# Performance work log

Hardware: AMD Instinct MI355X
Metric: run time of the kernel (lower is better)

## Reference

```python
import jax, jax.numpy as jnp
import numpy as np

B_SZ = 8
G = 2048
D_MODEL = 512
D_STATE = 128
D_CONV = 4
EXPAND = 2
HEADDIM = 64
D_INNER = EXPAND * D_MODEL          # 1024
NHEADS = D_INNER // HEADDIM         # 16
CONV_DIM = D_INNER + 2 * D_STATE    # 1280
D_IN_PROJ = 2 * D_INNER + 2 * D_STATE + NHEADS  # 2320
ID_DIM = 128
CHR_DIM = 64
N_CHR = 25
F_LOCUS = 32
PATH_DIM = 128
GENE_FEAT = ID_DIM + PATH_DIM + 2 * CHR_DIM  # 384
N_PERT = 10000
P_DIM = 128


def silu(x):
    return x * jax.nn.sigmoid(x)


def causal_dw_conv(x, w, b):
    # x: (B,L,C), w: (C,K), b: (C,)  causal depthwise conv (left pad K-1)
    K = w.shape[1]
    L = x.shape[1]
    xp = jnp.pad(x, ((0, 0), (K - 1, 0), (0, 0)))
    out = b[None, None, :]
    for k in range(K):
        out = out + xp[:, k:k + L, :] * w[:, k][None, None, :]
    return out


def mamba2(u, in_w, conv_w, conv_b, dt_bias, A_log, Dp, norm_w, out_w):
    # u: (B,L,d_model) -> (B,L,d_model); mamba_ssm Mamba2 defaults, ngroups=1
    Bb, L, _ = u.shape
    zxbcdt = u @ in_w.T                                   # (B,L,D_IN_PROJ)
    z = zxbcdt[..., :D_INNER]
    xBC = zxbcdt[..., D_INNER:D_INNER + CONV_DIM]
    dt = zxbcdt[..., D_INNER + CONV_DIM:]                 # (B,L,H)
    xBC = silu(causal_dw_conv(xBC, conv_w, conv_b))
    x = xBC[..., :D_INNER].reshape(Bb, L, NHEADS, HEADDIM)
    Bm = xBC[..., D_INNER:D_INNER + D_STATE]              # (B,L,N)
    Cm = xBC[..., D_INNER + D_STATE:]                     # (B,L,N)
    dt = jax.nn.softplus(dt + dt_bias)                    # (B,L,H)
    dA = jnp.exp(dt * (-jnp.exp(A_log)))                  # (B,L,H)

    def step(h, inp):
        dA_t, dt_t, B_t, C_t, x_t = inp
        h = dA_t[:, :, None, None] * h + jnp.einsum('bh,bn,bhp->bhpn', dt_t, B_t, x_t)
        y = jnp.einsum('bhpn,bn->bhp', h, C_t)
        return h, y

    h0 = jnp.zeros((Bb, NHEADS, HEADDIM, D_STATE), u.dtype)
    xs = (dA.transpose(1, 0, 2), dt.transpose(1, 0, 2),
          Bm.transpose(1, 0, 2), Cm.transpose(1, 0, 2), x.transpose(1, 0, 2, 3))
    _, ys = jax.lax.scan(step, h0, xs)                    # ys: (L,B,H,P)
    y = ys.transpose(1, 0, 2, 3) + Dp[None, None, :, None] * x
    y = y.reshape(Bb, L, D_INNER)
    # gated RMSNorm (norm_before_gate=False): norm(y * silu(z))
    y = y * silu(z)
    y = y * jax.lax.rsqrt(jnp.mean(y * y, axis=-1, keepdims=True) + 1e-5) * norm_w
    return y @ out_w.T


def setup_inputs() -> dict:
    key = jax.random.key(0)
    ks = iter(jax.random.split(key, 48))

    def nrm(shape, scale):
        return jax.random.normal(next(ks), shape, jnp.float32) * scale

    inp = {}
    inp['perturbation_idx'] = jax.random.randint(next(ks), (B_SZ,), 0, N_PERT)
    inp['chr_idx'] = jax.random.randint(next(ks), (G,), 0, N_CHR)
    inp['locus_fourier'] = nrm((G, 2 * F_LOCUS), 1.0)
    inp['pathway_features'] = nrm((G, PATH_DIM), 1.0)
    inp['pert_emb'] = nrm((N_PERT, P_DIM), 0.02)
    inp['gene_id_emb'] = nrm((G, ID_DIM), 0.02)
    inp['chr_emb'] = nrm((N_CHR, CHR_DIM), 0.02)
    inp['locus_w'] = nrm((CHR_DIM, 2 * F_LOCUS), (2 * F_LOCUS) ** -0.5)
    inp['locus_b'] = jnp.zeros((CHR_DIM,), jnp.float32)
    inp['cond_w'] = nrm((GENE_FEAT, P_DIM), P_DIM ** -0.5)
    inp['cond_b'] = jnp.zeros((GENE_FEAT,), jnp.float32)
    inp['in_w'] = nrm((D_MODEL, GENE_FEAT), GENE_FEAT ** -0.5)
    inp['in_b'] = jnp.zeros((D_MODEL,), jnp.float32)
    inp['head_w'] = nrm((1, D_MODEL), D_MODEL ** -0.5)
    inp['head_b'] = jnp.zeros((1,), jnp.float32)
    for p in ('f_', 'b_'):
        inp[p + 'in_w'] = nrm((D_IN_PROJ, D_MODEL), D_MODEL ** -0.5)
        inp[p + 'conv_w'] = nrm((CONV_DIM, D_CONV), D_CONV ** -0.5)
        inp[p + 'conv_b'] = jnp.zeros((CONV_DIM,), jnp.float32)
        inp[p + 'dt_bias'] = nrm((NHEADS,), 0.5)
        inp[p + 'A_log'] = jnp.log(jax.random.uniform(next(ks), (NHEADS,), jnp.float32, 1.0, 16.0))
        inp[p + 'D'] = jnp.ones((NHEADS,), jnp.float32)
        inp[p + 'norm_w'] = jnp.ones((D_INNER,), jnp.float32)
        inp[p + 'out_w'] = nrm((D_MODEL, D_INNER), D_INNER ** -0.5)
    return inp


def reference(perturbation_idx, chr_idx, locus_fourier, pathway_features,
              pert_emb, gene_id_emb, chr_emb, locus_w, locus_b,
              cond_w, cond_b, in_w, in_b, head_w, head_b,
              f_in_w, f_conv_w, f_conv_b, f_dt_bias, f_A_log, f_D, f_norm_w, f_out_w,
              b_in_w, b_conv_w, b_conv_b, b_dt_bias, b_A_log, b_D, b_norm_w, b_out_w):
    B = perturbation_idx.shape[0]
    cond = pert_emb[perturbation_idx] @ cond_w.T + cond_b          # (B, GENE_FEAT)
    e_chr = chr_emb[chr_idx]                                        # (G, CHR_DIM)
    e_locus = jax.nn.gelu(locus_fourier @ locus_w.T + locus_b, approximate=False)
    gene_feat = jnp.concatenate([gene_id_emb, pathway_features, e_chr, e_locus], axis=1)  # (G, GENE_FEAT)
    seq = jnp.concatenate([cond[:, None, :],
                           jnp.broadcast_to(gene_feat[None], (B,) + gene_feat.shape)], axis=1)
    seq = seq @ in_w.T + in_b                                       # (B, G+1, d_model)
    h_fwd = mamba2(seq, f_in_w, f_conv_w, f_conv_b, f_dt_bias, f_A_log, f_D, f_norm_w, f_out_w)
    h_bwd = jnp.flip(mamba2(jnp.flip(seq, axis=1), b_in_w, b_conv_w, b_conv_b,
                            b_dt_bias, b_A_log, b_D, b_norm_w, b_out_w), axis=1)
    H = h_fwd + h_bwd
    return H[:, 1:, :] @ head_w.T + head_b                          # (B, G, 1)
```

## Files before the change

### kernel.cpp

```cpp
#include <hip/hip_runtime.h>
#include <hip/hip_bf16.h>
#include <hip/hip_fp16.h>
#include <math.h>

#define DPROJ 2320
#define CONVD 1280

typedef __attribute__((ext_vector_type(8))) short bf16x8;
typedef __attribute__((ext_vector_type(4))) float f32x4;

__device__ __forceinline__ float siluf(float x) { return x / (1.f + __expf(-x)); }
__device__ __forceinline__ float bfu(unsigned short s) { return __uint_as_float(((unsigned)s) << 16); }
__device__ __forceinline__ unsigned short f2bf(float f) {
    unsigned u = __float_as_uint(f);
    unsigned r = (u + 0x7FFFu + ((u >> 16) & 1u)) >> 16;
    return (unsigned short)r;
}
__device__ __forceinline__ unsigned short f2h(float f) {
    __half h = __float2half(f);
    return *(unsigned short*)&h;
}
__device__ __forceinline__ float h2f(unsigned short s) {
    __half h = *(__half*)&s;
    return __half2float(h);
}


__global__ void gg_kernel(const int* __restrict__ chridx, const float* __restrict__ gid,
                          const float* __restrict__ path, const float* __restrict__ chrE,
                          const int* __restrict__ pidx, const float* __restrict__ pertE,
                          float* __restrict__ gf, float* __restrict__ cemb,
                          float* __restrict__ wf2, float* __restrict__ wb2) {
    int blk = blockIdx.x, tid = threadIdx.x;
    if (blk < 3072) {
        int idx = blk * 256 + tid;
        int g = idx / 384, j = idx % 384;
        float v;
        if (j < 128)      v = gid[(size_t)g * 128 + j];
        else if (j < 256) v = path[(size_t)g * 128 + (j - 128)];
        else if (j < 320) v = chrE[(size_t)chridx[g] * 64 + (j - 256)];
        else return;
        gf[idx] = v;
    } else if (blk < 3076) {
        int idx = (blk - 3072) * 256 + tid;
        int b = idx >> 7, k = idx & 127;
        cemb[idx] = pertE[(size_t)pidx[b] * 128 + k];
    } else {
        wf2[tid * 4 + 0] = 0.f; wf2[tid * 4 + 1] = 0.f;
        wf2[tid * 4 + 2] = 0.f; wf2[tid * 4 + 3] = 0.f;
        wb2[tid * 4 + 0] = 0.f; wb2[tid * 4 + 1] = 0.f;
        wb2[tid * 4 + 2] = 0.f; wb2[tid * 4 + 3] = 0.f;
    }
}

__global__ void wfold_kernel(const float* __restrict__ headW,
                             const float* __restrict__ fOutW, const float* __restrict__ fNw,
                             const float* __restrict__ bOutW, const float* __restrict__ bNw,
                             float* __restrict__ wf2, float* __restrict__ wb2) {
    int blk = blockIdx.x;
    int dir = blk >> 6;
    int rem = blk & 63;
    int dseg = rem >> 4, mseg = rem & 15;
    int tid = threadIdx.x;
    int d = dseg * 256 + tid;
    const float* W = dir ? bOutW : fOutW;
    float s = 0.f;
#pragma unroll
    for (int m = mseg * 32; m < mseg * 32 + 32; ++m)
        s += headW[m] * W[(size_t)m * 1024 + d];
    const float* nw = dir ? bNw : fNw;
    atomicAdd(&(dir ? wb2 : wf2)[d], s * nw[d]);
}


__global__ void tobf4_kernel(const float* __restrict__ inW, const float* __restrict__ fInW,
                             const float* __restrict__ bInW, const float* __restrict__ gf,
                             unsigned short* __restrict__ inW2, unsigned short* __restrict__ fInW2,
                             unsigned short* __restrict__ bInW2, unsigned short* __restrict__ gf2) {
    size_t idx = (size_t)blockIdx.x * 256 + threadIdx.x;
    const size_t A = 512UL * 384, B5 = 2432UL * 512;
    if (idx < A) {
        inW2[idx] = f2bf(inW[idx]);
    } else if (idx < A + B5) {
        size_t k = idx - A; int m = k / 512, kk = k % 512;
        fInW2[k] = f2bf(m < 2320 ? fInW[(size_t)m * 512 + kk] : 0.f);
    } else if (idx < A + 2 * B5) {
        size_t k = idx - A - B5; int m = k / 512, kk = k % 512;
        bInW2[k] = f2bf(m < 2320 ? bInW[(size_t)m * 512 + kk] : 0.f);
    } else {
        size_t k = idx - A - 2 * B5;
        gf2[k] = f2bf(gf[k]);
    }
}


__global__ __launch_bounds__(256) void mfma_gemm_kernel(
    const unsigned short* __restrict__ A2, const unsigned short* __restrict__ W2,
    const float* __restrict__ bias, unsigned short* __restrict__ Cbf,
    int N, int K2, int ldc) {
    __shared__ __align__(16) unsigned short Al[128 * 40];
    __shared__ __align__(16) unsigned short Bl[128 * 40];
    const int tid = threadIdx.x;
    const int bm = blockIdx.y * 128, bn = blockIdx.x * 128;
    const int lane = tid & 63, wave = tid >> 6;
    const int wm = (wave >> 1) * 64, wn = (wave & 1) * 64;
    f32x4 acc[4][4];
#pragma unroll
    for (int i = 0; i < 4; ++i)
#pragma unroll
        for (int j = 0; j < 4; ++j) acc[i][j] = (f32x4){0.f, 0.f, 0.f, 0.f};

    for (int k0 = 0; k0 < K2; k0 += 32) {
        __syncthreads();
#pragma unroll
        for (int s = 0; s < 2; ++s) {
            int ch = tid + 256 * s;
            int row = ch >> 2, q = ch & 3;
            uint4 va = *(const uint4*)&A2[(size_t)(bm + row) * K2 + k0 + q * 8];
            *(uint4*)&Al[row * 40 + q * 8] = va;
            uint4 vb = *(const uint4*)&W2[(size_t)(bn + row) * K2 + k0 + q * 8];
            *(uint4*)&Bl[row * 40 + q * 8] = vb;
        }
        __syncthreads();
        bf16x8 af[4], bfr[4];
#pragma unroll
        for (int i = 0; i < 4; ++i)
            af[i] = *(const bf16x8*)&Al[(wm + i * 16 + (lane & 15)) * 40 + (lane >> 4) * 8];
#pragma unroll
        for (int j = 0; j < 4; ++j)
            bfr[j] = *(const bf16x8*)&Bl[(wn + j * 16 + (lane & 15)) * 40 + (lane >> 4) * 8];
#pragma unroll
        for (int i = 0; i < 4; ++i)
#pragma unroll
            for (int j = 0; j < 4; ++j)
                acc[i][j] = __builtin_amdgcn_mfma_f32_16x16x32_bf16(af[i], bfr[j], acc[i][j], 0, 0, 0);
    }
#pragma unroll
    for (int i = 0; i < 4; ++i) {
        int m = bm + wm + i * 16 + (lane >> 4) * 4;
#pragma unroll
        for (int j = 0; j < 4; ++j) {
            int n = bn + wn + j * 16 + (lane & 15);
            if (n < N) {
                float bv = bias ? bias[n] : 0.f;
#pragma unroll
                for (int r = 0; r < 4; ++r)
                    Cbf[(size_t)(m + r) * ldc + n] = f2bf(acc[i][j][r] + bv);
            }
        }
    }
}


__global__ __launch_bounds__(256) void zx_gemm_kernel(
    const unsigned short* __restrict__ A2,
    const unsigned short* __restrict__ fInW2, const unsigned short* __restrict__ bInW2,
    unsigned short* __restrict__ szF, unsigned short* __restrict__ xbcF, float* __restrict__ dtrF,
    unsigned short* __restrict__ szB, unsigned short* __restrict__ xbcB, float* __restrict__ dtrB) {
    __shared__ __align__(16) unsigned short Al[128 * 40];
    __shared__ __align__(16) unsigned short Bl[128 * 40];
    const int tid = threadIdx.x;
    const int bxx = blockIdx.x;
    const int d = (bxx >= 19);
    const int bn = (d ? bxx - 19 : bxx) * 128, bm = blockIdx.y * 128;
    const unsigned short* W2 = d ? bInW2 : fInW2;
    unsigned short* sz = d ? szB : szF;
    unsigned short* xbc = d ? xbcB : xbcF;
    float* dtr = d ? dtrB : dtrF;
    const int lane = tid & 63, wave = tid >> 6;
    const int wm = (wave >> 1) * 64, wn = (wave & 1) * 64;
    const int K2 = 512, N = 2320;
    f32x4 acc[4][4];
#pragma unroll
    for (int i = 0; i < 4; ++i)
#pragma unroll
        for (int j = 0; j < 4; ++j) acc[i][j] = (f32x4){0.f, 0.f, 0.f, 0.f};

    for (int k0 = 0; k0 < K2; k0 += 32) {
        __syncthreads();
#pragma unroll
        for (int s = 0; s < 2; ++s) {
            int ch = tid + 256 * s;
            int row = ch >> 2, q = ch & 3;
            uint4 va = *(const uint4*)&A2[(size_t)(bm + row) * K2 + k0 + q * 8];
            *(uint4*)&Al[row * 40 + q * 8] = va;
            uint4 vb = *(const uint4*)&W2[(size_t)(bn + row) * K2 + k0 + q * 8];
            *(uint4*)&Bl[row * 40 + q * 8] = vb;
        }
        __syncthreads();
        bf16x8 af[4], bfr[4];
#pragma unroll
        for (int i = 0; i < 4; ++i)
            af[i] = *(const bf16x8*)&Al[(wm + i * 16 + (lane & 15)) * 40 + (lane >> 4) * 8];
#pragma unroll
        for (int j = 0; j < 4; ++j)
            bfr[j] = *(const bf16x8*)&Bl[(wn + j * 16 + (lane & 15)) * 40 + (lane >> 4) * 8];
#pragma unroll
        for (int i = 0; i < 4; ++i)
#pragma unroll
            for (int j = 0; j < 4; ++j)
                acc[i][j] = __builtin_amdgcn_mfma_f32_16x16x32_bf16(af[i], bfr[j], acc[i][j], 0, 0, 0);
    }
#pragma unroll
    for (int i = 0; i < 4; ++i) {
        int m = bm + wm + i * 16 + (lane >> 4) * 4;
#pragma unroll
        for (int j = 0; j < 4; ++j) {
            int n = bn + wn + j * 16 + (lane & 15);
            if (n < N) {
#pragma unroll
                for (int r = 0; r < 4; ++r) {
                    float v = acc[i][j][r];
                    if (n < 1024)
                        sz[(size_t)(m + r) * 1024 + n] = f2h(siluf(v));
                    else if (n < 2304)
                        xbc[(size_t)(m + r) * 1280 + (n - 1024)] = f2bf(v);
                    else
                        dtr[(size_t)(m + r) * 16 + (n - 2304)] = v;
                }
            }
        }
    }
}


__global__ __launch_bounds__(256) void gemm_kernel(
    const float* __restrict__ A, const float* __restrict__ W,
    const float* __restrict__ bias, float* __restrict__ C,
    int M, int N, int K, int ldc, int act) {
    __shared__ __align__(16) float As[16][68];
    __shared__ __align__(16) float Ws[16][68];
    const int tid = threadIdx.x;
    const int tx = tid & 15, ty = tid >> 4;
    const int bm = blockIdx.y * 64, bn = blockIdx.x * 64;
    const int lr = tid >> 2;
    const int lk = (tid & 3) * 4;
    float acc[4][4];
#pragma unroll
    for (int i = 0; i < 4; ++i)
#pragma unroll
        for (int j = 0; j < 4; ++j) acc[i][j] = 0.f;

    for (int k0 = 0; k0 < K; k0 += 16) {
        const int am = bm + lr;
        const int wn = bn + lr;
        float4 av = make_float4(0.f, 0.f, 0.f, 0.f), wv = make_float4(0.f, 0.f, 0.f, 0.f);
        if (am < M) av = *(const float4*)&A[(size_t)am * K + k0 + lk];
        if (wn < N) wv = *(const float4*)&W[(size_t)wn * K + k0 + lk];
        __syncthreads();
        As[lk + 0][lr] = av.x; As[lk + 1][lr] = av.y; As[lk + 2][lr] = av.z; As[lk + 3][lr] = av.w;
        Ws[lk + 0][lr] = wv.x; Ws[lk + 1][lr] = wv.y; Ws[lk + 2][lr] = wv.z; Ws[lk + 3][lr] = wv.w;
        __syncthreads();
#pragma unroll
        for (int kk = 0; kk < 16; ++kk) {
            float4 a = *(const float4*)&As[kk][ty * 4];
            float4 w = *(const float4*)&Ws[kk][tx * 4];
            float aa[4] = {a.x, a.y, a.z, a.w}, ww[4] = {w.x, w.y, w.z, w.w};
#pragma unroll
            for (int i = 0; i < 4; ++i)
#pragma unroll
                for (int j = 0; j < 4; ++j) acc[i][j] += aa[i] * ww[j];
        }
    }
#pragma unroll
    for (int i = 0; i < 4; ++i) {
        const int m = bm + ty * 4 + i;
        if (m >= M) continue;
#pragma unroll
        for (int j = 0; j < 4; ++j) {
            const int n = bn + tx * 4 + j;
            if (n >= N) continue;
            float v = acc[i][j] + (bias ? bias[n] : 0.f);
            if (act == 1) v = 0.5f * v * (1.f + erff(v * 0.70710678118654752f));
            C[(size_t)m * ldc + n] = v;
        }
    }
}


__global__ void dt_kernel(const float* __restrict__ dtrF, const float* __restrict__ dtrB,
                          const float* __restrict__ zxc,
                          const float* __restrict__ fDtB, const float* __restrict__ bDtB,
                          float* __restrict__ dtFsT, float* __restrict__ dtBsT,
                          float* __restrict__ dtFp) {
    int idx = blockIdx.x * 256 + threadIdx.x;
    if (idx < 32768) {
        int r = idx >> 4, hh = idx & 15;
        float raw = dtrF[idx] + fDtB[hh];
        dtFsT[hh * 2048 + r] = (raw > 20.f) ? raw : log1pf(expf(raw));
    } else if (idx < 65536) {
        int k = idx - 32768;
        int r = k >> 4, hh = k & 15;
        float raw = dtrB[(size_t)(2047 - r) * 16 + hh] + bDtB[hh];
        dtBsT[hh * 2048 + r] = (raw > 20.f) ? raw : log1pf(expf(raw));
    } else if (idx < 65664) {
        int k = idx - 65536;
        int b = k >> 4, hh = k & 15;
        float raw = zxc[(size_t)b * DPROJ + 2304 + hh] + fDtB[hh];
        dtFp[k] = (raw > 20.f) ? raw : log1pf(expf(raw));
    }
}

__global__ void cum_kernel(const float* __restrict__ dtFsT, const float* __restrict__ dtBsT,
                           const float* __restrict__ fAlog, const float* __restrict__ bAlog,
                           float* __restrict__ cumF, float* __restrict__ cumB) {
    int id = blockIdx.x * 256 + threadIdx.x;
    int dir = id >> 9, k = id & 511, h = k >> 5, c = k & 31;
    const float* dtT = dir ? dtBsT : dtFsT;
    const float* Al = dir ? bAlog : fAlog;
    float* cum = dir ? cumB : cumF;
    float a = -expf(Al[h]);
    float acc = 0.f;
    for (int s4 = 0; s4 < 16; ++s4) {
        float4 v = *(const float4*)&dtT[h * 2048 + c * 64 + s4 * 4];
        float4 o;
        acc += v.x * a; o.x = acc;
        acc += v.y * a; o.y = acc;
        acc += v.z * a; o.z = acc;
        acc += v.w * a; o.w = acc;
        *(float4*)&cum[h * 2048 + c * 64 + s4 * 4] = o;
    }
}


__global__ void conv_kernel(const unsigned short* __restrict__ xbcF,
                            const unsigned short* __restrict__ xbcB,
                            const float* __restrict__ zxc,
                            const float* __restrict__ fCw, const float* __restrict__ fCb,
                            const float* __restrict__ bCw, const float* __restrict__ bCb,
                            unsigned short* __restrict__ bcF, unsigned short* __restrict__ xF16,
                            unsigned short* __restrict__ bcB, unsigned short* __restrict__ xB16,
                            float* __restrict__ convFp, unsigned short* __restrict__ bcFp,
                            unsigned short* __restrict__ xFp16) {
    int blk = blockIdx.x, tid = threadIdx.x;
    if (blk < 10225) {
        int idx = blk * 256 + tid;
        if (idx >= 2045 * 1280) return;
        int t4 = idx / 1280, c = idx % 1280;
        float4 w4 = *(const float4*)&fCw[c * 4];
        float acc = fCb[c];
        acc += bfu(xbcF[(size_t)(t4 + 0) * 1280 + c]) * w4.x;
        acc += bfu(xbcF[(size_t)(t4 + 1) * 1280 + c]) * w4.y;
        acc += bfu(xbcF[(size_t)(t4 + 2) * 1280 + c]) * w4.z;
        acc += bfu(xbcF[(size_t)(t4 + 3) * 1280 + c]) * w4.w;
        float r = siluf(acc);
        if (c >= 1024) bcF[(size_t)t4 * 256 + (c - 1024)] = f2bf(r);
        else           xF16[(size_t)t4 * 1024 + c] = f2bf(r);
    } else if (blk < 20465) {
        int idx = (blk - 10225) * 256 + tid;
        int s = idx / 1280, c = idx % 1280;
        float4 w4 = *(const float4*)&bCw[c * 4];
        float w[4] = {w4.x, w4.y, w4.z, w4.w};
        float acc = bCb[c];
#pragma unroll
        for (int k = 0; k < 4; ++k) {
            int j = s - 3 + k;
            if (j >= 0) acc += bfu(xbcB[(size_t)(2047 - j) * 1280 + c]) * w[k];
        }
        float r = siluf(acc);
        if (c >= 1024) bcB[(size_t)s * 256 + (c - 1024)] = f2bf(r);
        else           xB16[(size_t)s * 1024 + c] = f2bf(r);
    } else {
        int idx = (blk - 20465) * 256 + tid;
        int b = idx / 5120;
        int r = idx % 5120;
        int t = r / 1280, c = r % 1280;
        float4 w4 = *(const float4*)&fCw[c * 4];
        float w[4] = {w4.x, w4.y, w4.z, w4.w};
        float acc = fCb[c];
#pragma unroll
        for (int k = 0; k < 4; ++k) {
            int j = t - 3 + k;
            float x = 0.f;
            if (j == 0)      x = zxc[(size_t)b * DPROJ + 1024 + c];
            else if (j >= 1) x = bfu(xbcF[(size_t)(j - 1) * 1280 + c]);
            acc += x * w[k];
        }
        float rr = siluf(acc);
        convFp[idx] = rr;
        if (c >= 1024) bcFp[(size_t)(b * 4 + t) * 256 + (c - 1024)] = f2bf(rr);
        else           xFp16[(size_t)(b * 4 + t) * 1024 + c] = f2bf(rr);
    }
}


__global__ __launch_bounds__(256) void intra_kernel(
    const unsigned short* __restrict__ bcF, const unsigned short* __restrict__ bcFp,
    const unsigned short* __restrict__ bcB,
    const unsigned short* __restrict__ xF16, const unsigned short* __restrict__ xFp16,
    const unsigned short* __restrict__ xB16,
    const float* __restrict__ dtFsT, const float* __restrict__ dtBsT,
    const float* __restrict__ cumF, const float* __restrict__ cumB,
    unsigned short* __restrict__ YiF0, unsigned short* __restrict__ YiFs,
    unsigned short* __restrict__ YiB,
    unsigned short* __restrict__ UF0, unsigned short* __restrict__ UFs,
    unsigned short* __restrict__ UB) {
    __shared__ __align__(16) unsigned char smraw[63232];
    unsigned short* Bt = (unsigned short*)smraw;
    unsigned short* Ct = (unsigned short*)(smraw + 17408);
    unsigned short* Sm = (unsigned short*)(smraw + 17408);
    unsigned short* BT = (unsigned short*)(smraw + 34816);
    unsigned short* XT = (unsigned short*)(smraw + 53248);
    float* scum = (float*)(smraw + 62464);
    float* sdt  = scum + 64;
    float* se   = scum + 128;

    const int iid = blockIdx.x;
    int dir, b = 0, h, c;
    unsigned short *Yout, *Uout;
    if (iid < 128)      { dir = 0; b = iid >> 4; h = iid & 15; c = 0;
                          Yout = YiF0 + (size_t)(b * 16 + h) * 4096; Uout = UF0 + (size_t)(b * 16 + h) * 8192; }
    else if (iid < 624) { int k = iid - 128; dir = 0; c = 1 + (k >> 4); h = k & 15;
                          Yout = YiFs + (size_t)(c * 16 + h) * 4096; Uout = UFs + (size_t)(c * 16 + h) * 8192; }
    else                { int k = iid - 624; dir = 1; c = k >> 4; h = k & 15;
                          Yout = YiB + (size_t)(c * 16 + h) * 4096;  Uout = UB + (size_t)(c * 16 + h) * 8192; }
    const float* dtAT = dir ? dtBsT : dtFsT;
    const float* cumA = dir ? cumB : cumF;

    const int tid = threadIdx.x;
    const int lane = tid & 63, wave = tid >> 6;
    const int quad = lane >> 4, l15 = lane & 15;

    {
        int r = tid >> 2, q = tid & 3;
        const unsigned short *bsrc, *xsrc;
        if (dir == 0) {
            int t = 64 * c + 1 + r;
            if (t < 4) { bsrc = bcFp + (size_t)(b * 4 + t) * 256; xsrc = xFp16 + (size_t)(b * 4 + t) * 1024; }
            else       { bsrc = bcF + (size_t)(t - 4) * 256;      xsrc = xF16 + (size_t)(t - 4) * 1024; }
        } else {
            int s = 64 * c + r;
            bsrc = bcB + (size_t)s * 256;
            xsrc = xB16 + (size_t)s * 1024;
        }
#pragma unroll
        for (int i = 0; i < 4; ++i) {
            int n0 = q * 32 + i * 8;
            uint4 v = *(const uint4*)&bsrc[n0];
            *(uint4*)&Bt[r * 136 + n0] = v;
            const unsigned short* pv = (const unsigned short*)&v;
#pragma unroll
            for (int jj = 0; jj < 8; ++jj) BT[(n0 + jj) * 72 + r] = pv[jj];
        }
#pragma unroll
        for (int i = 0; i < 4; ++i) {
            int n0 = q * 32 + i * 8;
            uint4 v = *(const uint4*)&bsrc[128 + n0];
            *(uint4*)&Ct[r * 136 + n0] = v;
        }
#pragma unroll
        for (int k = 0; k < 2; ++k) {
            uint4 v = *(const uint4*)&xsrc[h * 64 + q * 16 + k * 8];
            const unsigned short* pv = (const unsigned short*)&v;
#pragma unroll
            for (int jj = 0; jj < 8; ++jj) XT[(q * 16 + k * 8 + jj) * 72 + r] = pv[jj];
        }
        if (tid < 64) {
            int j = 64 * c + tid;
            scum[tid] = cumA[h * 2048 + j];
            sdt[tid] = dtAT[h * 2048 + j];
        }
    }
    __syncthreads();
    if (tid < 64) se[tid] = __expf(scum[63] - scum[tid]) * sdt[tid];

    const int tm = (wave >> 1) * 32, sn = (wave & 1) * 32;
    f32x4 acc1[2][2];
#pragma unroll
    for (int i = 0; i < 2; ++i)
#pragma unroll
        for (int j = 0; j < 2; ++j) acc1[i][j] = (f32x4){0.f, 0.f, 0.f, 0.f};
#pragma unroll
    for (int ks = 0; ks < 4; ++ks) {
        bf16x8 af[2], bfr[2];
#pragma unroll
        for (int i = 0; i < 2; ++i)
            af[i] = *(const bf16x8*)&Ct[(tm + i * 16 + l15) * 136 + ks * 32 + quad * 8];
#pragma unroll
        for (int j = 0; j < 2; ++j)
            bfr[j] = *(const bf16x8*)&Bt[(sn + j * 16 + l15) * 136 + ks * 32 + quad * 8];
#pragma unroll
        for (int i = 0; i < 2; ++i)
#pragma unroll
            for (int j = 0; j < 2; ++j)
                acc1[i][j] = __builtin_amdgcn_mfma_f32_16x16x32_bf16(af[i], bfr[j], acc1[i][j], 0, 0, 0);
    }
    __syncthreads();

#pragma unroll
    for (int j = 0; j < 2; ++j) {
        int s = sn + j * 16 + l15;
        float cs = scum[s], ds = sdt[s];
#pragma unroll
        for (int i = 0; i < 2; ++i) {
#pragma unroll
            for (int r = 0; r < 4; ++r) {
                int t = tm + i * 16 + quad * 4 + r;
                float v = (s <= t) ? __expf(scum[t] - cs) * ds * acc1[i][j][r] : 0.f;
                Sm[t * 72 + s] = f2bf(v);
            }
        }
    }
    __syncthreads();

    const int pm = (wave >> 1) * 32, tn = (wave & 1) * 32;
    f32x4 acc2[2][2];
#pragma unroll
    for (int i = 0; i < 2; ++i)
#pragma unroll
        for (int j = 0; j < 2; ++j) acc2[i][j] = (f32x4){0.f, 0.f, 0.f, 0.f};
#pragma unroll
    for (int ks = 0; ks < 2; ++ks) {
        bf16x8 af[2], bfr[2];
#pragma unroll
        for (int i = 0; i < 2; ++i)
            af[i] = *(const bf16x8*)&XT[(pm + i * 16 + l15) * 72 + ks * 32 + quad * 8];
#pragma unroll
        for (int j = 0; j < 2; ++j)
            bfr[j] = *(const bf16x8*)&Sm[(tn + j * 16 + l15) * 72 + ks * 32 + quad * 8];
#pragma unroll
        for (int i = 0; i < 2; ++i)
#pragma unroll
            for (int j = 0; j < 2; ++j)
                acc2[i][j] = __builtin_amdgcn_mfma_f32_16x16x32_bf16(af[i], bfr[j], acc2[i][j], 0, 0, 0);
    }
#pragma unroll
    for (int i = 0; i < 2; ++i)
#pragma unroll
        for (int j = 0; j < 2; ++j) {
            int t = tn + j * 16 + l15;
            int p0 = pm + i * 16 + quad * 4;
            ushort4 o = make_ushort4(f2bf(acc2[i][j][0]), f2bf(acc2[i][j][1]),
                                     f2bf(acc2[i][j][2]), f2bf(acc2[i][j][3]));
            *(ushort4*)&Yout[t * 64 + p0] = o;
        }

    const int nm = wave * 32;
    f32x4 acc3[2][4];
#pragma unroll
    for (int i = 0; i < 2; ++i)
#pragma unroll
        for (int j = 0; j < 4; ++j) acc3[i][j] = (f32x4){0.f, 0.f, 0.f, 0.f};
#pragma unroll
    for (int ks = 0; ks < 2; ++ks) {
        float ev[8];
#pragma unroll
        for (int jj = 0; jj < 8; ++jj) ev[jj] = se[ks * 32 + quad * 8 + jj];
        bf16x8 bfx[4];
#pragma unroll
        for (int j = 0; j < 4; ++j) {
            bf16x8 xs = *(const bf16x8*)&XT[(j * 16 + l15) * 72 + ks * 32 + quad * 8];
#pragma unroll
            for (int jj = 0; jj < 8; ++jj)
                bfx[j][jj] = (short)f2bf(bfu((unsigned short)xs[jj]) * ev[jj]);
        }
        bf16x8 af[2];
#pragma unroll
        for (int i = 0; i < 2; ++i)
            af[i] = *(const bf16x8*)&BT[(nm + i * 16 + l15) * 72 + ks * 32 + quad * 8];
#pragma unroll
        for (int i = 0; i < 2; ++i)
#pragma unroll
            for (int j = 0; j < 4; ++j)
                acc3[i][j] = __builtin_amdgcn_mfma_f32_16x16x32_bf16(af[i], bfx[j], acc3[i][j], 0, 0, 0);
    }
#pragma unroll
    for (int i = 0; i < 2; ++i)
#pragma unroll
        for (int j = 0; j < 4; ++j) {
            int p = j * 16 + l15;
            int n0 = nm + i * 16 + quad * 4;
            ushort4 o = make_ushort4(f2bf(acc3[i][j][0]), f2bf(acc3[i][j][1]),
                                     f2bf(acc3[i][j][2]), f2bf(acc3[i][j][3]));
            *(ushort4*)&Uout[p * 128 + n0] = o;
        }
}


__global__ void mid_kernel(const float* __restrict__ convFp, const unsigned short* __restrict__ bcF,
                           const float* __restrict__ dtFp, const float* __restrict__ cumF,
                           const float* __restrict__ cumB,
                           const unsigned short* __restrict__ UF0,
                           const unsigned short* __restrict__ UFs, const unsigned short* __restrict__ UB,
                           float* __restrict__ cb0, unsigned short* __restrict__ Mb,
                           unsigned short* __restrict__ Tst, float* __restrict__ psiF) {
    int blk = blockIdx.x, tid = threadIdx.x;
    if (blk < 32) {
        int idx = blk * 256 + tid;
        int b = idx >> 10, r = idx & 1023, h = r >> 6, tl = r & 63;
        int t = tl + 1;
        const float* b0 = convFp + (size_t)(b * 4) * CONVD;
        float s = 0.f;
        if (t < 4) {
            const float* crow = convFp + (size_t)(b * 4 + t) * CONVD;
            for (int n = 0; n < 128; ++n) s += crow[1152 + n] * b0[1024 + n];
        } else {
            const unsigned short* cr = bcF + (size_t)(t - 4) * 256 + 128;
            for (int n = 0; n < 128; ++n) s += bfu(cr[n]) * b0[1024 + n];
        }
        cb0[(b * 16 + h) * 64 + tl] = s * dtFp[b * 16 + h];
    } else if (blk < 160) {
        int bh = blk - 32;
        int b = bh >> 4, h = bh & 15;
        float D0 = __expf(cumF[h * 2048 + 63]);
        float dt0 = dtFp[b * 16 + h];
        const float* row0 = convFp + (size_t)(b * 4) * CONVD;
        const unsigned short* u = UF0 + (size_t)(b * 16 + h) * 8192;
        unsigned short* m = Mb + (size_t)(b * 16 + h) * 8192;
        for (int e4 = tid; e4 < 2048; e4 += 256) {
            int e = e4 * 4, p = e >> 7, n0 = e & 127;
            float s = D0 * dt0 * row0[h * 64 + p];
            float4 B4 = *(const float4*)&row0[1024 + n0];
            ushort4 uv = *(const ushort4*)&u[e];
            ushort4 o = make_ushort4(f2bf(s * B4.x + bfu(uv.x)), f2bf(s * B4.y + bfu(uv.y)),
                                     f2bf(s * B4.z + bfu(uv.z)), f2bf(s * B4.w + bfu(uv.w)));
            *(ushort4*)&m[e] = o;
        }
    } else {
        int blk2 = blk - 160;
        int dir = blk2 >> 7, h = (blk2 >> 3) & 15, q8 = blk2 & 7;
        const unsigned short* U = dir ? UB : UFs;
        const float* cum = dir ? cumB : cumF;
        unsigned short* T = Tst + (size_t)(dir * 16 + h) * 32 * 8192;
        if (dir == 0 && q8 == 0 && tid == 0) {
            float ps = 1.f;
            for (int c = 1; c < 32; ++c) {
                psiF[h * 32 + c] = ps;
                ps *= __expf(cumF[h * 2048 + c * 64 + 63]);
            }
        }
        const size_t e = (size_t)q8 * 1024 + 4 * tid;
        float4 st = make_float4(0.f, 0.f, 0.f, 0.f);
        const int c0 = dir ? 0 : 1;
        ushort4 u = *(const ushort4*)&U[((size_t)c0 * 16 + h) * 8192 + e];
        for (int c = c0; c < 32; ++c) {
            ushort4 un = make_ushort4(0, 0, 0, 0);
            if (c + 1 < 32) un = *(const ushort4*)&U[((size_t)(c + 1) * 16 + h) * 8192 + e];
            float Dc = __expf(cum[h * 2048 + c * 64 + 63]);
            ushort4 o = make_ushort4(f2bf(st.x), f2bf(st.y), f2bf(st.z), f2bf(st.w));
            *(ushort4*)&T[(size_t)c * 8192 + e] = o;
            st.x = Dc * st.x + bfu(u.x);
            st.y = Dc * st.y + bfu(u.y);
            st.z = Dc * st.z + bfu(u.z);
            st.w = Dc * st.w + bfu(u.w);
            u = un;
        }
    }
}


__global__ __launch_bounds__(256) void yt_kernel(
    const unsigned short* __restrict__ bcF, const unsigned short* __restrict__ bcB,
    const unsigned short* __restrict__ Tst,
    const unsigned short* __restrict__ YiFs, const unsigned short* __restrict__ YiB,
    const float* __restrict__ cumF, const float* __restrict__ cumB,
    unsigned short* __restrict__ YsF, unsigned short* __restrict__ YsB) {
    const int iid = blockIdx.x;
    int dir, h, c;
    if (iid < 496) { dir = 0; c = 1 + (iid >> 4); h = iid & 15; }
    else           { int k = iid - 496; dir = 1; c = k >> 4; h = k & 15; }
    const unsigned short* Cbase = (dir == 0)
        ? bcF + ((size_t)(64 * c - 3)) * 256 + 128
        : bcB + ((size_t)(64 * c)) * 256 + 128;
    const unsigned short* Tp = Tst + ((size_t)(dir * 16 + h) * 32 + c) * 8192;
    const unsigned short* Yi = (dir == 0 ? YiFs : YiB) + (size_t)(c * 16 + h) * 4096;
    const float* cum = dir ? cumB : cumF;
    unsigned short* Ys = (dir == 0 ? YsF : YsB) + (size_t)(c * 16 + h) * 4096;
    const int tid = threadIdx.x;
    const int lane = tid & 63, wave = tid >> 6;
    const int quad = lane >> 4, l15 = lane & 15;
    const int pm = (wave >> 1) * 32, tb = (wave & 1) * 32;
    f32x4 acc[2][2];
#pragma unroll
    for (int i = 0; i < 2; ++i)
#pragma unroll
        for (int j = 0; j < 2; ++j) acc[i][j] = (f32x4){0.f, 0.f, 0.f, 0.f};
#pragma unroll
    for (int ks = 0; ks < 4; ++ks) {
        bf16x8 af[2], bfr[2];
#pragma unroll
        for (int i = 0; i < 2; ++i)
            af[i] = *(const bf16x8*)&Tp[(size_t)(pm + i * 16 + l15) * 128 + ks * 32 + quad * 8];
#pragma unroll
        for (int j = 0; j < 2; ++j)
            bfr[j] = *(const bf16x8*)&Cbase[(size_t)(tb + j * 16 + l15) * 256 + ks * 32 + quad * 8];
#pragma unroll
        for (int i = 0; i < 2; ++i)
#pragma unroll
            for (int j = 0; j < 2; ++j)
                acc[i][j] = __builtin_amdgcn_mfma_f32_16x16x32_bf16(af[i], bfr[j], acc[i][j], 0, 0, 0);
    }
#pragma unroll
    for (int i = 0; i < 2; ++i)
#pragma unroll
        for (int j = 0; j < 2; ++j) {
            int t = tb + j * 16 + l15;
            int p0 = pm + i * 16 + quad * 4;
            float et = __expf(cum[h * 2048 + 64 * c + t]);
            ushort4 yi = *(const ushort4*)&Yi[t * 64 + p0];
            ushort4 o = make_ushort4(f2bf(bfu(yi.x) + et * acc[i][j][0]),
                                     f2bf(bfu(yi.y) + et * acc[i][j][1]),
                                     f2bf(bfu(yi.z) + et * acc[i][j][2]),
                                     f2bf(bfu(yi.w) + et * acc[i][j][3]));
            *(ushort4*)&Ys[t * 64 + p0] = o;
        }
}


__global__ __launch_bounds__(256) void gate_kernel(
    const unsigned short* __restrict__ bcF,
    const unsigned short* __restrict__ Mb, const float* __restrict__ psiF,
    const unsigned short* __restrict__ YsF, const unsigned short* __restrict__ YsB,
    const unsigned short* __restrict__ xF16, const unsigned short* __restrict__ xFp16,
    const unsigned short* __restrict__ xB16,
    const unsigned short* __restrict__ szF, const unsigned short* __restrict__ szB,
    const float* __restrict__ convFp,
    const float* __restrict__ cumF,
    const unsigned short* __restrict__ YiF0,
    const float* __restrict__ cb0,
    const float* __restrict__ fD, const float* __restrict__ bD,
    const float* __restrict__ wf2, const float* __restrict__ wb2,
    float* __restrict__ aF, float* __restrict__ aB) {
    __shared__ __align__(16) float Ysm[64 * 68];

    const int iid = blockIdx.x;
    int dir, b = 0, h, cg;
    if (iid < 1024) { dir = 0; b = iid >> 7; int r = iid & 127; h = r >> 3; cg = r & 7; }
    else            { int k = iid - 1024; dir = 1; h = k >> 3; cg = k & 7; }
    const int tid = threadIdx.x, tx = tid & 15, ty = tid >> 4;
    const int lane = tid & 63, wave = tid >> 6;
    const int quad = lane >> 4, l15 = lane & 15;

    const float Dh = (dir ? bD : fD)[h];
    const float* wvp = dir ? wb2 : wf2;
    float4 wreg = *(const float4*)&wvp[h * 64 + tx * 4];

    const int pm = (wave >> 1) * 32, tb = (wave & 1) * 32;
    bf16x8 mfr[4][2];
    if (dir == 0) {
        const unsigned short* Mp = Mb + (size_t)(b * 16 + h) * 8192;
#pragma unroll
        for (int ks = 0; ks < 4; ++ks)
#pragma unroll
            for (int i = 0; i < 2; ++i)
                mfr[ks][i] = *(const bf16x8*)&Mp[(size_t)(pm + i * 16 + l15) * 128 + ks * 32 + quad * 8];
    }

    for (int cc = 0; cc < 4; ++cc) {
        const int c = cg * 4 + cc;
        const bool fwdG = (dir == 0 && c > 0);
        if (fwdG) {
            if (cc > 0) __syncthreads();
            const unsigned short* Cbase = bcF + ((size_t)(64 * c - 3)) * 256 + 128;
            f32x4 acc[2][2];
#pragma unroll
            for (int i = 0; i < 2; ++i)
#pragma unroll
                for (int j = 0; j < 2; ++j) acc[i][j] = (f32x4){0.f, 0.f, 0.f, 0.f};
#pragma unroll
            for (int ks = 0; ks < 4; ++ks) {
                bf16x8 bfr[2];
#pragma unroll
                for (int j = 0; j < 2; ++j)
                    bfr[j] = *(const bf16x8*)&Cbase[(size_t)(tb + j * 16 + l15) * 256 + ks * 32 + quad * 8];
#pragma unroll
                for (int i = 0; i < 2; ++i)
#pragma unroll
                    for (int j = 0; j < 2; ++j)
                        acc[i][j] = __builtin_amdgcn_mfma_f32_16x16x32_bf16(mfr[ks][i], bfr[j], acc[i][j], 0, 0, 0);
            }
#pragma unroll
            for (int i = 0; i < 2; ++i)
#pragma unroll
                for (int j = 0; j < 2; ++j)
                    *(f32x4*)&Ysm[(tb + j * 16 + l15) * 68 + pm + i * 16 + quad * 4] = acc[i][j];
            __syncthreads();
        }

        const float psi = fwdG ? psiF[h * 32 + c] : 0.f;
        float4 x0v = make_float4(0.f, 0.f, 0.f, 0.f);
        float cbv[4] = {0.f, 0.f, 0.f, 0.f};
        if (dir == 0 && c == 0) {
            x0v = *(const float4*)&convFp[(size_t)(b * 4) * CONVD + h * 64 + tx * 4];
#pragma unroll
            for (int i = 0; i < 4; ++i) cbv[i] = cb0[(b * 16 + h) * 64 + (ty + 16 * i)];
        }

        float rawet[4];
        ushort4 y4a[4], x4a[4], z4a[4];
        float4 cm4a[4];
#pragma unroll
        for (int i = 0; i < 4; ++i) {
            int tl = ty + 16 * i;
            int j = 64 * c + tl;
            rawet[i] = (dir == 0) ? cumF[h * 2048 + j] : 0.f;
            const unsigned short *Yp, *xp, *zp;
            if (dir == 0) {
                Yp = (c == 0) ? YiF0 + (size_t)(b * 16 + h) * 4096 : YsF + (size_t)(c * 16 + h) * 4096;
                if (c == 0) {
                    int t = j + 1;
                    xp = (t < 4) ? xFp16 + (size_t)(b * 4 + t) * 1024 : xF16 + (size_t)(t - 4) * 1024;
                } else {
                    xp = xF16 + (size_t)(64 * c + tl - 3) * 1024;
                }
                zp = szF + (size_t)j * 1024;
            } else {
                Yp = YsB + (size_t)(c * 16 + h) * 4096;
                xp = xB16 + (size_t)j * 1024;
                zp = szB + (size_t)(2047 - j) * 1024;
            }
            y4a[i] = *(const ushort4*)&Yp[tl * 64 + tx * 4];
            x4a[i] = *(const ushort4*)&xp[h * 64 + tx * 4];
            z4a[i] = *(const ushort4*)&zp[h * 64 + tx * 4];
            if (fwdG)                    cm4a[i] = *(const float4*)&Ysm[tl * 68 + tx * 4];
            else if (dir == 0 && c == 0) cm4a[i] = x0v;
            else                         cm4a[i] = make_float4(0.f, 0.f, 0.f, 0.f);
        }

#pragma unroll
        for (int i = 0; i < 4; ++i) {
            int j = 64 * c + ty + 16 * i;
            float k1 = 0.f;
            if (dir == 0) {
                float et = __expf(rawet[i]);
                k1 = (c == 0) ? et * cbv[i] : et * psi;
            }
            float yv[4] = {bfu(y4a[i].x), bfu(y4a[i].y), bfu(y4a[i].z), bfu(y4a[i].w)};
            float xa[4] = {bfu(x4a[i].x), bfu(x4a[i].y), bfu(x4a[i].z), bfu(x4a[i].w)};
            float sza[4] = {h2f(z4a[i].x), h2f(z4a[i].y), h2f(z4a[i].z), h2f(z4a[i].w)};
            float cma[4] = {cm4a[i].x, cm4a[i].y, cm4a[i].z, cm4a[i].w};
            float wa[4] = {wreg.x, wreg.y, wreg.z, wreg.w};
            float a1 = 0.f, a2 = 0.f;
#pragma unroll
            for (int w = 0; w < 4; ++w) {
                float tot = yv[w] + k1 * cma[w] + Dh * xa[w];
                float g = tot * sza[w];
                a1 += g * wa[w];
                a2 += g * g;
            }
#pragma unroll
            for (int m = 1; m < 16; m <<= 1) {
                a1 += __shfl_xor(a1, m);
                a2 += __shfl_xor(a2, m);
            }
            if (tx == 0) {
                if (dir == 0) {
                    size_t o = ((size_t)(b * 2048 + j) * 16 + h) * 2;
                    aF[o] = a1; aF[o + 1] = a2;
                } else {
                    int g = 2047 - j;
                    size_t o = ((size_t)g * 16 + h) * 2;
                    aB[o] = a1; aB[o + 1] = a2;
                }
            }
        }
    }
}


__global__ void final_kernel(const float* __restrict__ aF, const float* __restrict__ aB,
                             const float* __restrict__ headB, float* __restrict__ out) {
    int idx = blockIdx.x * 256 + threadIdx.x;
    int b = idx >> 11, g = idx & 2047;
    const float* pf = aF + ((size_t)(b * 2048 + g)) * 32;
    const float* pb = aB + (size_t)g * 32;
    float f1 = 0.f, f2 = 0.f, b1 = 0.f, b2 = 0.f;
#pragma unroll
    for (int h = 0; h < 16; ++h) {
        f1 += pf[2 * h]; f2 += pf[2 * h + 1];
        b1 += pb[2 * h]; b2 += pb[2 * h + 1];
    }
    out[idx] = f1 * rsqrtf(f2 * (1.f / 1024.f) + 1e-5f) +
               b1 * rsqrtf(b2 * (1.f / 1024.f) + 1e-5f) + headB[0];
}


extern "C" void kernel_launch(void* const* d_in, const int* in_sizes, int n_in,
                              void* d_out, int out_size, void* d_ws, size_t ws_size,
                              hipStream_t stream) {
    const int*   pidx   = (const int*)  d_in[0];
    const int*   chridx = (const int*)  d_in[1];
    const float* locusF = (const float*)d_in[2];
    const float* pathF  = (const float*)d_in[3];
    const float* pertE  = (const float*)d_in[4];
    const float* gidE   = (const float*)d_in[5];
    const float* chrE   = (const float*)d_in[6];
    const float* locusW = (const float*)d_in[7];
    const float* locusB = (const float*)d_in[8];
    const float* condW  = (const float*)d_in[9];
    const float* condB  = (const float*)d_in[10];
    const float* inW    = (const float*)d_in[11];
    const float* inB    = (const float*)d_in[12];
    const float* headW  = (const float*)d_in[13];
    const float* headB  = (const float*)d_in[14];
    const float* fInW   = (const float*)d_in[15];
    const float* fCw    = (const float*)d_in[16];
    const float* fCb    = (const float*)d_in[17];
    const float* fDtB   = (const float*)d_in[18];
    const float* fAlog  = (const float*)d_in[19];
    const float* fDp    = (const float*)d_in[20];
    const float* fNw    = (const float*)d_in[21];
    const float* fOutW  = (const float*)d_in[22];
    const float* bInW   = (const float*)d_in[23];
    const float* bCw    = (const float*)d_in[24];
    const float* bCb    = (const float*)d_in[25];
    const float* bDtB   = (const float*)d_in[26];
    const float* bAlog  = (const float*)d_in[27];
    const float* bDp    = (const float*)d_in[28];
    const float* bNw    = (const float*)d_in[29];
    const float* bOutW  = (const float*)d_in[30];
    float* out = (float*)d_out;
    (void)in_sizes; (void)n_in; (void)out_size; (void)ws_size;

    char* base = (char*)d_ws;
    size_t off = 0;
    auto allocf = [&](size_t n) -> float* {
        char* r = base + off; off += ((n * 4 + 63) & ~(size_t)63); return (float*)r; };
    auto allocu = [&](size_t n) -> unsigned short* {
        char* r = base + off; off += ((n * 2 + 63) & ~(size_t)63); return (unsigned short*)r; };

    float* gf     = allocf(2048UL * 384);
    float* cond   = allocf(8UL * 384);
    float* cemb   = allocf(8UL * 128);
    float* uc     = allocf(8UL * 512);
    float* zxc    = allocf(8UL * DPROJ);
    float* convFp = allocf(8UL * 4 * CONVD);
    float* dtrF   = allocf(2048UL * 16);
    float* dtrB   = allocf(2048UL * 16);
    float* dtFsT  = allocf(16UL * 2048);
    float* dtFp   = allocf(128);
    float* dtBsT  = allocf(16UL * 2048);
    float* cumF   = allocf(16UL * 2048);
    float* cumB   = allocf(16UL * 2048);
    float* wf2    = allocf(1024);
    float* wb2    = allocf(1024);
    float* cb0    = allocf(8UL * 16 * 64);
    float* psiF   = allocf(16UL * 32);
    float* aF     = allocf(8UL * 2048 * 16 * 2);
    float* aB     = allocf(2048UL * 16 * 2);
    unsigned short* xbcF = allocu(2048UL * 1280);
    unsigned short* xbcB = allocu(2048UL * 1280);
    unsigned short* YiF0 = allocu(8UL * 16 * 4096);
    unsigned short* YiFs = allocu(32UL * 16 * 4096);
    unsigned short* YiB  = allocu(32UL * 16 * 4096);
    unsigned short* UF0  = allocu(8UL * 16 * 8192);
    unsigned short* UFs  = allocu(32UL * 16 * 8192);
    unsigned short* UB   = allocu(32UL * 16 * 8192);
    unsigned short* Mb   = allocu(8UL * 16 * 8192);
    unsigned short* Tst  = allocu(2UL * 16 * 32 * 8192);
    unsigned short* bcF  = allocu(2045UL * 256);
    unsigned short* bcFp = allocu(32UL * 256);
    unsigned short* bcB  = allocu(2048UL * 256);
    unsigned short* YsF  = allocu(32UL * 16 * 4096);
    unsigned short* YsB  = allocu(32UL * 16 * 4096);
    unsigned short* xF16 = allocu(2045UL * 1024);
    unsigned short* xFp16= allocu(32UL * 1024);
    unsigned short* xB16 = allocu(2048UL * 1024);
    unsigned short* szF  = allocu(2048UL * 1024);
    unsigned short* szB  = allocu(2048UL * 1024);
    unsigned short* gf2   = allocu(2048UL * 384);
    unsigned short* inW2  = allocu(512UL * 384);
    unsigned short* ug2   = allocu(2048UL * 512);
    unsigned short* fInW2 = allocu(2432UL * 512);
    unsigned short* bInW2 = allocu(2432UL * 512);

    gg_kernel<<<3077, 256, 0, stream>>>(chridx, gidE, pathF, chrE, pidx, pertE, gf, cemb, wf2, wb2);
    wfold_kernel<<<128, 256, 0, stream>>>(headW, fOutW, fNw, bOutW, bNw, wf2, wb2);
    gemm_kernel<<<dim3(1, 32), 256, 0, stream>>>(locusF, locusW, locusB, gf + 320, 2048, 64, 64, 384, 1);
    gemm_kernel<<<dim3(6, 1), 256, 0, stream>>>(cemb, condW, condB, cond, 8, 384, 128, 384, 0);

    tobf4_kernel<<<13568, 256, 0, stream>>>(inW, fInW, bInW, gf, inW2, fInW2, bInW2, gf2);

    mfma_gemm_kernel<<<dim3(4, 16), 256, 0, stream>>>(gf2, inW2, inB, ug2, 512, 384, 512);
    gemm_kernel<<<dim3(8, 1), 256, 0, stream>>>(cond, inW, inB, uc, 8, 512, 384, 512, 0);

    zx_gemm_kernel<<<dim3(38, 16), 256, 0, stream>>>(ug2, fInW2, bInW2,
                                                     szF, xbcF, dtrF, szB, xbcB, dtrB);
    gemm_kernel<<<dim3(37, 1), 256, 0, stream>>>(uc, fInW, nullptr, zxc, 8, DPROJ, 512, DPROJ, 0);

    dt_kernel<<<257, 256, 0, stream>>>(dtrF, dtrB, zxc, fDtB, bDtB, dtFsT, dtBsT, dtFp);
    cum_kernel<<<4, 256, 0, stream>>>(dtFsT, dtBsT, fAlog, bAlog, cumF, cumB);
    conv_kernel<<<20625, 256, 0, stream>>>(xbcF, xbcB, zxc, fCw, fCb, bCw, bCb,
                                           bcF, xF16, bcB, xB16, convFp, bcFp, xFp16);
    intra_kernel<<<1136, 256, 0, stream>>>(bcF, bcFp, bcB, xF16, xFp16, xB16,
                                           dtFsT, dtBsT, cumF, cumB,
                                           YiF0, YiFs, YiB, UF0, UFs, UB);
    mid_kernel<<<416, 256, 0, stream>>>(convFp, bcF, dtFp, cumF, cumB, UF0, UFs, UB,
                                        cb0, Mb, Tst, psiF);
    yt_kernel<<<1008, 256, 0, stream>>>(bcF, bcB, Tst, YiFs, YiB, cumF, cumB, YsF, YsB);
    gate_kernel<<<1152, 256, 0, stream>>>(bcF, Mb, psiF, YsF, YsB, xF16, xFp16, xB16,
                                          szF, szB, convFp, cumF,
                                          YiF0, cb0, fDp, bDp, wf2, wb2, aF, aB);
    final_kernel<<<64, 256, 0, stream>>>(aF, aB, headB, out);
}
```

Measured before the change: 372.9 us.

## Fold D*x skip term into yt_kernel and split gate_kernel into more blocks

The D*x skip contribution for batch-independent chunks (all backward chunks and forward chunks c>0) is now added once in yt_kernel, which is shared across the batch. gate_kernel no longer re-reads x for those chunks in every batch. gate_kernel also processes 2 chunks per block instead of 4, doubling the grid to 2304 blocks, and issues its global loads before the MFMA/LDS phase so their latency can overlap. Tradeoffs are an extra bf16 rounding of the combined term, since it is folded in before the store, and more per-block setup such as the M fragment loads being repeated.

```diff
diff --git a/kernel.cpp b/kernel.cpp
--- a/kernel.cpp
+++ b/kernel.cpp
@@ -653,7 +653,9 @@
     const unsigned short* __restrict__ bcF, const unsigned short* __restrict__ bcB,
     const unsigned short* __restrict__ Tst,
     const unsigned short* __restrict__ YiFs, const unsigned short* __restrict__ YiB,
+    const unsigned short* __restrict__ xF16, const unsigned short* __restrict__ xB16,
     const float* __restrict__ cumF, const float* __restrict__ cumB,
+    const float* __restrict__ fD, const float* __restrict__ bD,
     unsigned short* __restrict__ YsF, unsigned short* __restrict__ YsB) {
     const int iid = blockIdx.x;
     int dir, h, c;
@@ -664,7 +666,10 @@
         : bcB + ((size_t)(64 * c)) * 256 + 128;
     const unsigned short* Tp = Tst + ((size_t)(dir * 16 + h) * 32 + c) * 8192;
     const unsigned short* Yi = (dir == 0 ? YiFs : YiB) + (size_t)(c * 16 + h) * 4096;
+    const unsigned short* xbase = (dir == 0) ? xF16 + ((size_t)(64 * c - 3)) * 1024
+                                             : xB16 + ((size_t)(64 * c)) * 1024;
     const float* cum = dir ? cumB : cumF;
+    const float Dh = (dir ? bD : fD)[h];
     unsigned short* Ys = (dir == 0 ? YsF : YsB) + (size_t)(c * 16 + h) * 4096;
     const int tid = threadIdx.x;
     const int lane = tid & 63, wave = tid >> 6;
@@ -698,10 +703,11 @@
             int p0 = pm + i * 16 + quad * 4;
             float et = __expf(cum[h * 2048 + 64 * c + t]);
             ushort4 yi = *(const ushort4*)&Yi[t * 64 + p0];
-            ushort4 o = make_ushort4(f2bf(bfu(yi.x) + et * acc[i][j][0]),
-                                     f2bf(bfu(yi.y) + et * acc[i][j][1]),
-                                     f2bf(bfu(yi.z) + et * acc[i][j][2]),
-                                     f2bf(bfu(yi.w) + et * acc[i][j][3]));
+            ushort4 xv = *(const ushort4*)&xbase[(size_t)t * 1024 + h * 64 + p0];
+            ushort4 o = make_ushort4(f2bf(bfu(yi.x) + et * acc[i][j][0] + Dh * bfu(xv.x)),
+                                     f2bf(bfu(yi.y) + et * acc[i][j][1] + Dh * bfu(xv.y)),
+                                     f2bf(bfu(yi.z) + et * acc[i][j][2] + Dh * bfu(xv.z)),
+                                     f2bf(bfu(yi.w) + et * acc[i][j][3] + Dh * bfu(xv.w)));
             *(ushort4*)&Ys[t * 64 + p0] = o;
         }
 }
@@ -712,26 +718,25 @@
     const unsigned short* __restrict__ Mb, const float* __restrict__ psiF,
     const unsigned short* __restrict__ YsF, const unsigned short* __restrict__ YsB,
     const unsigned short* __restrict__ xF16, const unsigned short* __restrict__ xFp16,
-    const unsigned short* __restrict__ xB16,
     const unsigned short* __restrict__ szF, const unsigned short* __restrict__ szB,
     const float* __restrict__ convFp,
     const float* __restrict__ cumF,
     const unsigned short* __restrict__ YiF0,
     const float* __restrict__ cb0,
-    const float* __restrict__ fD, const float* __restrict__ bD,
+    const float* __restrict__ fD,
     const float* __restrict__ wf2, const float* __restrict__ wb2,
     float* __restrict__ aF, float* __restrict__ aB) {
     __shared__ __align__(16) float Ysm[64 * 68];
 
     const int iid = blockIdx.x;
     int dir, b = 0, h, cg;
-    if (iid < 1024) { dir = 0; b = iid >> 7; int r = iid & 127; h = r >> 3; cg = r & 7; }
-    else            { int k = iid - 1024; dir = 1; h = k >> 3; cg = k & 7; }
+    if (iid < 2048) { dir = 0; b = iid >> 8; int r = iid & 255; h = r >> 4; cg = r & 15; }
+    else            { int k = iid - 2048; dir = 1; h = k >> 4; cg = k & 15; }
     const int tid = threadIdx.x, tx = tid & 15, ty = tid >> 4;
     const int lane = tid & 63, wave = tid >> 6;
     const int quad = lane >> 4, l15 = lane & 15;
 
-    const float Dh = (dir ? bD : fD)[h];
+    const float Dh = dir ? 0.f : fD[h];
     const float* wvp = dir ? wb2 : wf2;
     float4 wreg = *(const float4*)&wvp[h * 64 + tx * 4];
 
@@ -746,9 +751,45 @@
                 mfr[ks][i] = *(const bf16x8*)&Mp[(size_t)(pm + i * 16 + l15) * 128 + ks * 32 + quad * 8];
     }
 
-    for (int cc = 0; cc < 4; ++cc) {
-        const int c = cg * 4 + cc;
+    for (int cc = 0; cc < 2; ++cc) {
+        const int c = cg * 2 + cc;
         const bool fwdG = (dir == 0 && c > 0);
+        const bool c0 = (dir == 0 && c == 0);
+
+        float rawet[4];
+        ushort4 y4a[4], z4a[4], x4a[4];
+#pragma unroll
+        for (int i = 0; i < 4; ++i) {
+            int tl = ty + 16 * i;
+            int j = 64 * c + tl;
+            rawet[i] = (dir == 0) ? cumF[h * 2048 + j] : 0.f;
+            const unsigned short *Yp, *zp;
+            if (dir == 0) {
+                Yp = c0 ? YiF0 + (size_t)(b * 16 + h) * 4096 : YsF + (size_t)(c * 16 + h) * 4096;
+                zp = szF + (size_t)j * 1024;
+            } else {
+                Yp = YsB + (size_t)(c * 16 + h) * 4096;
+                zp = szB + (size_t)(2047 - j) * 1024;
+            }
+            y4a[i] = *(const ushort4*)&Yp[tl * 64 + tx * 4];
+            z4a[i] = *(const ushort4*)&zp[h * 64 + tx * 4];
+            if (c0) {
+                int t = j + 1;
+                const unsigned short* xp = (t < 4) ? xFp16 + (size_t)(b * 4 + t) * 1024
+                                                   : xF16 + (size_t)(t - 4) * 1024;
+                x4a[i] = *(const ushort4*)&xp[h * 64 + tx * 4];
+            } else {
+                x4a[i] = make_ushort4(0, 0, 0, 0);
+            }
+        }
+        float4 x0v = make_float4(0.f, 0.f, 0.f, 0.f);
+        float cbv[4] = {0.f, 0.f, 0.f, 0.f};
+        if (c0) {
+            x0v = *(const float4*)&convFp[(size_t)(b * 4) * CONVD + h * 64 + tx * 4];
+#pragma unroll
+            for (int i = 0; i < 4; ++i) cbv[i] = cb0[(b * 16 + h) * 64 + (ty + 16 * i)];
+        }
+
         if (fwdG) {
             if (cc > 0) __syncthreads();
             const unsigned short* Cbase = bcF + ((size_t)(64 * c - 3)) * 256 + 128;
@@ -778,62 +819,31 @@
         }
 
         const float psi = fwdG ? psiF[h * 32 + c] : 0.f;
-        float4 x0v = make_float4(0.f, 0.f, 0.f, 0.f);
-        float cbv[4] = {0.f, 0.f, 0.f, 0.f};
-        if (dir == 0 && c == 0) {
-            x0v = *(const float4*)&convFp[(size_t)(b * 4) * CONVD + h * 64 + tx * 4];
-#pragma unroll
-            for (int i = 0; i < 4; ++i) cbv[i] = cb0[(b * 16 + h) * 64 + (ty + 16 * i)];
-        }
-
-        float rawet[4];
-        ushort4 y4a[4], x4a[4], z4a[4];
-        float4 cm4a[4];
+
 #pragma unroll
         for (int i = 0; i < 4; ++i) {
             int tl = ty + 16 * i;
             int j = 64 * c + tl;
-            rawet[i] = (dir == 0) ? cumF[h * 2048 + j] : 0.f;
-            const unsigned short *Yp, *xp, *zp;
-            if (dir == 0) {
-                Yp = (c == 0) ? YiF0 + (size_t)(b * 16 + h) * 4096 : YsF + (size_t)(c * 16 + h) * 4096;
-                if (c == 0) {
-                    int t = j + 1;
-                    xp = (t < 4) ? xFp16 + (size_t)(b * 4 + t) * 1024 : xF16 + (size_t)(t - 4) * 1024;
-                } else {
-                    xp = xF16 + (size_t)(64 * c + tl - 3) * 1024;
-                }
-                zp = szF + (size_t)j * 1024;
-            } else {
-                Yp = YsB + (size_t)(c * 16 + h) * 4096;
-                xp = xB16 + (size_t)j * 1024;
-                zp = szB + (size_t)(2047 - j) * 1024;
-            }
-            y4a[i] = *(const ushort4*)&Yp[tl * 64 + tx * 4];
-            x4a[i] = *(const ushort4*)&xp[h * 64 + tx * 4];
-            z4a[i] = *(const ushort4*)&zp[h * 64 + tx * 4];
-            if (fwdG)                    cm4a[i] = *(const float4*)&Ysm[tl * 68 + tx * 4];
-            else if (dir == 0 && c == 0) cm4a[i] = x0v;
-            else                         cm4a[i] = make_float4(0.f, 0.f, 0.f, 0.f);
-        }
-
-#pragma unroll
-        for (int i = 0; i < 4; ++i) {
-            int j = 64 * c + ty + 16 * i;
             float k1 = 0.f;
-            if (dir == 0) {
+            float cma[4] = {0.f, 0.f, 0.f, 0.f};
+            if (fwdG) {
                 float et = __expf(rawet[i]);
-                k1 = (c == 0) ? et * cbv[i] : et * psi;
+                k1 = et * psi;
+                float4 cmv = *(const float4*)&Ysm[tl * 68 + tx * 4];
+                cma[0] = cmv.x; cma[1] = cmv.y; cma[2] = cmv.z; cma[3] = cmv.w;
+            } else if (c0) {
+                float et = __expf(rawet[i]);
+                k1 = et * cbv[i];
+                cma[0] = x0v.x; cma[1] = x0v.y; cma[2] = x0v.z; cma[3] = x0v.w;
             }
             float yv[4] = {bfu(y4a[i].x), bfu(y4a[i].y), bfu(y4a[i].z), bfu(y4a[i].w)};
+            float sza[4] = {h2f(z4a[i].x), h2f(z4a[i].y), h2f(z4a[i].z), h2f(z4a[i].w)};
             float xa[4] = {bfu(x4a[i].x), bfu(x4a[i].y), bfu(x4a[i].z), bfu(x4a[i].w)};
-            float sza[4] = {h2f(z4a[i].x), h2f(z4a[i].y), h2f(z4a[i].z), h2f(z4a[i].w)};
-            float cma[4] = {cm4a[i].x, cm4a[i].y, cm4a[i].z, cm4a[i].w};
             float wa[4] = {wreg.x, wreg.y, wreg.z, wreg.w};
             float a1 = 0.f, a2 = 0.f;
 #pragma unroll
             for (int w = 0; w < 4; ++w) {
-                float tot = yv[w] + k1 * cma[w] + Dh * xa[w];
+                float tot = yv[w] + k1 * cma[w] + (c0 ? Dh * xa[w] : 0.f);
                 float g = tot * sza[w];
                 a1 += g * wa[w];
                 a2 += g * g;
@@ -987,9 +997,10 @@
                                            YiF0, YiFs, YiB, UF0, UFs, UB);
     mid_kernel<<<416, 256, 0, stream>>>(convFp, bcF, dtFp, cumF, cumB, UF0, UFs, UB,
                                         cb0, Mb, Tst, psiF);
-    yt_kernel<<<1008, 256, 0, stream>>>(bcF, bcB, Tst, YiFs, YiB, cumF, cumB, YsF, YsB);
-    gate_kernel<<<1152, 256, 0, stream>>>(bcF, Mb, psiF, YsF, YsB, xF16, xFp16, xB16,
+    yt_kernel<<<1008, 256, 0, stream>>>(bcF, bcB, Tst, YiFs, YiB, xF16, xB16,
+                                        cumF, cumB, fDp, bDp, YsF, YsB);
+    gate_kernel<<<2304, 256, 0, stream>>>(bcF, Mb, psiF, YsF, YsB, xF16, xFp16,
                                           szF, szB, convFp, cumF,
-                                          YiF0, cb0, fDp, bDp, wf2, wb2, aF, aB);
+                                          YiF0, cb0, fDp, wf2, wb2, aF, aB);
     final_kernel<<<64, 256, 0, stream>>>(aF, aB, headB, out);
 }
```

Result: no change. 366.4 us (-1.8%).
